# Performance work log

Measured on AMD Instinct MI355X. Metric: run time of the kernel, lower is better.

## Reference

```python
import jax, jax.numpy as jnp
import numpy as np

B, S, T, D, H, DF, E = 16, 1024, 512, 512, 8, 2048, 4
DH = D // H
EPS = 1e-5


def setup_inputs() -> dict:
    key = jax.random.key(0)
    ks = iter(jax.random.split(key, 64))

    def nrm(shape, scale=0.02):
        return jax.random.normal(next(ks), shape, dtype=jnp.float32) * scale

    inp = {
        "x": jax.random.normal(next(ks), (B, S, D), dtype=jnp.float32),
        "cross": jax.random.normal(next(ks), (B, T, D), dtype=jnp.float32),
    }
    for p in ("sa", "ca"):
        for w in ("wq", "wk", "wv", "wo"):
            inp[f"{p}_{w}"] = nrm((D, D))
            inp[f"{p}_b{w[1]}"] = jnp.zeros((D,), jnp.float32)
    inp["gate_w"] = nrm((D, E))
    inp["gate_b"] = jnp.zeros((E,), jnp.float32)
    inp["exp_w1"] = nrm((E, D, DF))
    inp["exp_b1"] = jnp.zeros((E, DF), jnp.float32)
    inp["exp_w2"] = nrm((E, DF, D))
    inp["exp_b2"] = jnp.zeros((E, D), jnp.float32)
    for i in (1, 2, 3):
        inp[f"n{i}_g"] = jnp.ones((D,), jnp.float32)
        inp[f"n{i}_b"] = jnp.zeros((D,), jnp.float32)
    return inp


def layer_norm(x, g, b):
    m = x.mean(-1, keepdims=True)
    v = x.var(-1, keepdims=True)
    return (x - m) * jax.lax.rsqrt(v + EPS) * g + b


def mha(q_in, kv_in, wq, bq, wk, bk, wv, bv, wo, bo, causal):
    Bq, Sq, _ = q_in.shape
    Sk = kv_in.shape[1]
    q = (q_in @ wq + bq).reshape(Bq, Sq, H, DH)
    k = (kv_in @ wk + bk).reshape(Bq, Sk, H, DH)
    v = (kv_in @ wv + bv).reshape(Bq, Sk, H, DH)
    scores = jnp.einsum('bshd,bthd->bhst', q, k) / jnp.sqrt(jnp.float32(DH))
    if causal:
        mask = jnp.tril(jnp.ones((Sq, Sk), dtype=bool))
        scores = jnp.where(mask, scores, jnp.float32(-1e9))
    attn = jax.nn.softmax(scores, axis=-1)
    out = jnp.einsum('bhst,bthd->bshd', attn, v).reshape(Bq, Sq, D)
    return out @ wo + bo


def moe_ffn(x, gw, gb, w1, b1, w2, b2):
    gates = jax.nn.softmax(x @ gw + gb, axis=-1)            # [B,S,E]
    h = jax.nn.relu(jnp.einsum('bsd,edf->bsef', x, w1) + b1)  # [B,S,E,DF]
    yo = jnp.einsum('bsef,efd->bsed', h, w2) + b2            # [B,S,E,D]
    y = jnp.einsum('bse,bsed->bsd', gates, yo)
    imp = gates.mean((0, 1))                                 # importance per expert
    aux = jnp.float32(E) * jnp.sum(imp * imp)                # load-balance penalty
    return y, aux


def reference(x, cross,
              sa_wq, sa_bq, sa_wk, sa_bk, sa_wv, sa_bv, sa_wo, sa_bo,
              ca_wq, ca_bq, ca_wk, ca_bk, ca_wv, ca_bv, ca_wo, ca_bo,
              gate_w, gate_b, exp_w1, exp_b1, exp_w2, exp_b2,
              n1_g, n1_b, n2_g, n2_b, n3_g, n3_b):
    # dropout is identity in eval mode
    x = x + mha(x, x, sa_wq, sa_bq, sa_wk, sa_bk, sa_wv, sa_bv, sa_wo, sa_bo, causal=True)
    x = layer_norm(x, n1_g, n1_b)
    x = x + mha(x, cross, ca_wq, ca_bq, ca_wk, ca_bk, ca_wv, ca_bv, ca_wo, ca_bo, causal=False)
    x = layer_norm(x, n2_g, n2_b)
    y, aux_loss = moe_ffn(x, gate_w, gate_b, exp_w1, exp_b1, exp_w2, exp_b2)
    out = layer_norm(x + y, n3_g, n3_b)
    return out, aux_loss
```

## Files before the change

kernel.cpp:

```cpp
#include <hip/hip_runtime.h>
#include <stdint.h>
#include <stddef.h>

typedef unsigned short bf16u;
typedef __attribute__((ext_vector_type(8))) short short8;
typedef __attribute__((ext_vector_type(4))) float f32x4;

__device__ __forceinline__ bf16u f2bf(float f) {
  union { float f; unsigned u; } v; v.f = f;
  unsigned r = v.u + 0x7FFFu + ((v.u >> 16) & 1u);
  return (bf16u)(r >> 16);
}

#define GL16(g, l) __builtin_amdgcn_global_load_lds( \
    (const __attribute__((address_space(1))) unsigned int*)(g), \
    (__attribute__((address_space(3))) unsigned int*)(l), 16, 0, 0)

enum { EPI_BF16 = 0, EPI_RELU_GATE = 1, EPI_VT = 2, EPI_RES = 3, EPI_ACC = 4 };

template<int EPI>
__global__ __launch_bounds__(256, 2) void gemm_k(
    const bf16u* __restrict__ A, const bf16u* __restrict__ BT,
    const float* __restrict__ bias, const float* __restrict__ res,
    const float* __restrict__ gates,
    bf16u* __restrict__ outb, float* __restrict__ outf,
    int M, int N, int K, int slog, int egate, int firste)
{
  __shared__ bf16u Ab[2][128 * 32];
  __shared__ bf16u Bb[2][128 * 32];
  const int tid = threadIdx.x, lane = tid & 63, w = tid >> 6;
  const int wm = w >> 1, wn = w & 1;
  const int nbt = N >> 7;
  const int mt = blockIdx.x / nbt, nt = blockIdx.x - mt * nbt;
  const int bm = mt << 7, bn = nt << 7;

  const int srow = lane >> 2;
  const int scol = (lane & 3) << 3;
  const bf16u* ap0 = A + (size_t)(bm + w * 16 + srow) * K + scol;
  const bf16u* ap1 = ap0 + (size_t)64 * K;
  const bf16u* bp0 = BT + (size_t)(bn + w * 16 + srow) * K + scol;
  const bf16u* bp1 = bp0 + (size_t)64 * K;

  f32x4 acc[4][4] = {};
  const int NT = K >> 5;

  GL16(ap0, &Ab[0][w * 512]);
  GL16(ap1, &Ab[0][(4 + w) * 512]);
  GL16(bp0, &Bb[0][w * 512]);
  GL16(bp1, &Bb[0][(4 + w) * 512]);
  __syncthreads();

  const int rl = lane & 15, kg = (lane >> 4) << 3;
  int cur = 0;
  for (int kt = 0; kt < NT; ++kt) {
    if (kt + 1 < NT) {
      const int ko = (kt + 1) << 5;
      const int nb = cur ^ 1;
      GL16(ap0 + ko, &Ab[nb][w * 512]);
      GL16(ap1 + ko, &Ab[nb][(4 + w) * 512]);
      GL16(bp0 + ko, &Bb[nb][w * 512]);
      GL16(bp1 + ko, &Bb[nb][(4 + w) * 512]);
    }
    short8 af[4], bfv[4];
    #pragma unroll
    for (int i = 0; i < 4; ++i)
      af[i] = *(const short8*)&Ab[cur][(wm * 64 + i * 16 + rl) * 32 + kg];
    #pragma unroll
    for (int j = 0; j < 4; ++j)
      bfv[j] = *(const short8*)&Bb[cur][(wn * 64 + j * 16 + rl) * 32 + kg];
    #pragma unroll
    for (int i = 0; i < 4; ++i)
      #pragma unroll
      for (int j = 0; j < 4; ++j)
        acc[i][j] = __builtin_amdgcn_mfma_f32_16x16x32_bf16(af[i], bfv[j], acc[i][j], 0, 0, 0);
    __syncthreads();
    cur ^= 1;
  }

  const int r0 = bm + wm * 64, c0 = bn + wn * 64;
  const int rsub = (lane >> 4) << 2;
  #pragma unroll
  for (int j = 0; j < 4; ++j) {
    const int col = c0 + j * 16 + rl;
    const float bs = bias ? bias[col] : 0.f;
    #pragma unroll
    for (int i = 0; i < 4; ++i) {
      const f32x4 v = acc[i][j];
      #pragma unroll
      for (int jj = 0; jj < 4; ++jj) {
        const int row = r0 + i * 16 + rsub + jj;
        float val = v[jj] + bs;
        if (EPI == EPI_BF16) {
          outb[(size_t)row * N + col] = f2bf(val);
        } else if (EPI == EPI_RELU_GATE) {
          const float g = gates[(size_t)row * 4 + egate];
          outb[(size_t)row * N + col] = f2bf(g * (val > 0.f ? val : 0.f));
        } else if (EPI == EPI_VT) {
          const int b_ = row >> slog, t_ = row & ((1 << slog) - 1);
          outb[(((size_t)(b_ * 8 + (col >> 6)) << 6) + (size_t)(col & 63)) * ((size_t)1 << slog) + t_] = f2bf(val);
        } else if (EPI == EPI_RES) {
          outf[(size_t)row * N + col] = res[(size_t)row * N + col] + val;
        } else {
          const size_t oi = (size_t)row * N + col;
          outf[oi] = firste ? val : (outf[oi] + val);
        }
      }
    }
  }
}

template<bool CAUSAL>
__global__ __launch_bounds__(256, 4) void attn_k(
    const bf16u* __restrict__ Q, const bf16u* __restrict__ Kg,
    const bf16u* __restrict__ VT, bf16u* __restrict__ O,
    int Sq, int Sk)
{
  __shared__ bf16u Kl[2][64 * 64];
  __shared__ bf16u Vl[2][64 * 64];
  __shared__ bf16u Pl[64 * 64];
  const int nqt = Sq >> 6;
  const int bh = blockIdx.x / nqt, qt = blockIdx.x - bh * nqt;
  const int b = bh >> 3, h = bh & 7;
  const int tid = threadIdx.x, lane = tid & 63, w = tid >> 6;
  const int rl = lane & 15, g4 = lane >> 4;

  const int qrow = qt * 64 + w * 16 + rl;
  const bf16u* qp = Q + (size_t)(b * Sq + qrow) * 512 + h * 64 + g4 * 8;
  const short8 qf0 = *(const short8*)qp;
  const short8 qf1 = *(const short8*)(qp + 32);

  f32x4 oacc[4] = {};
  float ml = -1e30f, ll = 0.f;
  const int KT = CAUSAL ? (qt + 1) : (Sk >> 6);

  const int str = tid >> 2, stc = tid & 3;
  const int sw_st = (str & 7) << 4;
  const bf16u* kq = Kg + (size_t)(b * Sk + str) * 512 + h * 64 + stc * 8;
  const bf16u* vq = VT + (size_t)(bh * 64 + str) * Sk + stc * 8;
  const int lo0 = str * 128 + ((stc * 16) ^ sw_st);
  const int lo1 = str * 128 + ((stc * 16 + 64) ^ sw_st);

  const int qr = w * 16 + rl;
  char* const pbase = (char*)Pl + qr * 128;
  const int swq = (qr & 7) << 4;

  {
    const short8 k0 = *(const short8*)kq;
    const short8 k1 = *(const short8*)(kq + 32);
    const short8 v0 = *(const short8*)vq;
    const short8 v1 = *(const short8*)(vq + 32);
    *(short8*)((char*)Kl[0] + lo0) = k0;
    *(short8*)((char*)Kl[0] + lo1) = k1;
    *(short8*)((char*)Vl[0] + lo0) = v0;
    *(short8*)((char*)Vl[0] + lo1) = v1;
  }
  __syncthreads();

  int cur = 0;
  for (int kt = 0; kt < KT; ++kt) {
    short8 nk0, nk1, nv0, nv1;
    const bool pre = (kt + 1 < KT);
    if (pre) {
      const bf16u* ks = kq + (size_t)(kt + 1) * 64 * 512;
      const bf16u* vs = vq + (kt + 1) * 64;
      nk0 = *(const short8*)ks;
      nk1 = *(const short8*)(ks + 32);
      nv0 = *(const short8*)vs;
      nv1 = *(const short8*)(vs + 32);
    }

    const bf16u* Kc = Kl[cur];
    const bf16u* Vc = Vl[cur];
    f32x4 st[4] = {};
    #pragma unroll
    for (int mi = 0; mi < 4; ++mi) {
      const int kr = mi * 16 + rl;
      const char* kb_ = (const char*)Kc + kr * 128;
      const int sw = (kr & 7) << 4;
      const short8 kf0 = *(const short8*)(kb_ + ((g4 * 16) ^ sw));
      const short8 kf1 = *(const short8*)(kb_ + ((g4 * 16 + 64) ^ sw));
      st[mi] = __builtin_amdgcn_mfma_f32_16x16x32_bf16(kf0, qf0, st[mi], 0, 0, 0);
      st[mi] = __builtin_amdgcn_mfma_f32_16x16x32_bf16(kf1, qf1, st[mi], 0, 0, 0);
    }

    const float SC = 0.125f * 1.44269504f;
    float sv[16];
    float pm = -1e30f;
    if (CAUSAL && kt == qt) {
      const int qg = qt * 64 + qr;
      #pragma unroll
      for (int mi = 0; mi < 4; ++mi)
        #pragma unroll
        for (int jj = 0; jj < 4; ++jj) {
          float s = st[mi][jj] * SC;
          const int kgi = kt * 64 + mi * 16 + g4 * 4 + jj;
          if (kgi > qg) s = -1e30f;
          sv[mi * 4 + jj] = s;
          pm = fmaxf(pm, s);
        }
    } else {
      #pragma unroll
      for (int mi = 0; mi < 4; ++mi)
        #pragma unroll
        for (int jj = 0; jj < 4; ++jj) {
          const float s = st[mi][jj] * SC;
          sv[mi * 4 + jj] = s;
          pm = fmaxf(pm, s);
        }
    }
    pm = fmaxf(pm, __shfl_xor(pm, 16));
    pm = fmaxf(pm, __shfl_xor(pm, 32));
    const float mnew = fmaxf(ml, pm);
    const float alpha = exp2f(ml - mnew);
    float ps = 0.f;
    bf16u pb[16];
    #pragma unroll
    for (int ii = 0; ii < 16; ++ii) {
      const float p = exp2f(sv[ii] - mnew);
      ps += p;
      pb[ii] = f2bf(p);
    }
    ps += __shfl_xor(ps, 16);
    ps += __shfl_xor(ps, 32);
    ll = ll * alpha + ps;
    ml = mnew;

    #pragma unroll
    for (int jj = 0; jj < 4; ++jj) {
      const float aj = __shfl(alpha, g4 * 4 + jj);
      #pragma unroll
      for (int ni = 0; ni < 4; ++ni) oacc[ni][jj] *= aj;
    }

    #pragma unroll
    for (int mi = 0; mi < 4; ++mi) {
      #pragma unroll
      for (int jp = 0; jp < 2; ++jp) {
        const unsigned pk = (unsigned)pb[mi * 4 + jp * 2] | ((unsigned)pb[mi * 4 + jp * 2 + 1] << 16);
        const int kx2 = mi * 32 + g4 * 8 + jp * 4;
        *(unsigned*)(pbase + (kx2 ^ swq)) = pk;
      }
    }
    asm volatile("s_waitcnt lgkmcnt(0)" ::: "memory");
    #pragma unroll
    for (int ks = 0; ks < 2; ++ks) {
      const short8 pf = *(const short8*)(pbase + ((g4 * 16 + ks * 64) ^ swq));
      #pragma unroll
      for (int ni = 0; ni < 4; ++ni) {
        const int vr = ni * 16 + rl;
        const short8 vf = *(const short8*)((const char*)Vc + vr * 128 + ((g4 * 16 + ks * 64) ^ ((vr & 7) << 4)));
        oacc[ni] = __builtin_amdgcn_mfma_f32_16x16x32_bf16(pf, vf, oacc[ni], 0, 0, 0);
      }
    }

    __syncthreads();
    if (pre) {
      const int nb = cur ^ 1;
      *(short8*)((char*)Kl[nb] + lo0) = nk0;
      *(short8*)((char*)Kl[nb] + lo1) = nk1;
      *(short8*)((char*)Vl[nb] + lo0) = nv0;
      *(short8*)((char*)Vl[nb] + lo1) = nv1;
      __syncthreads();
    }
    cur ^= 1;
  }

  #pragma unroll
  for (int jj = 0; jj < 4; ++jj) {
    const float lj = __shfl(ll, g4 * 4 + jj);
    const float inv = 1.f / lj;
    const int row = qt * 64 + w * 16 + g4 * 4 + jj;
    #pragma unroll
    for (int ni = 0; ni < 4; ++ni)
      O[(size_t)(b * Sq + row) * 512 + h * 64 + ni * 16 + rl] = f2bf(oacc[ni][jj] * inv);
  }
}

template<bool ADD, bool BOUT>
__global__ __launch_bounds__(256, 4) void ln_k(
    const float* __restrict__ X, const float* __restrict__ Y,
    const float* __restrict__ gam, const float* __restrict__ bet,
    float* __restrict__ outf, bf16u* __restrict__ outb)
{
  const int row = blockIdx.x * 4 + (threadIdx.x >> 6);
  const int lane = threadIdx.x & 63;
  const float* xp = X + (size_t)row * 512 + lane * 8;
  float v[8];
  {
    const float4 t0 = *(const float4*)xp;
    const float4 t1 = *(const float4*)(xp + 4);
    v[0] = t0.x; v[1] = t0.y; v[2] = t0.z; v[3] = t0.w;
    v[4] = t1.x; v[5] = t1.y; v[6] = t1.z; v[7] = t1.w;
  }
  if (ADD) {
    const float* yp = Y + (size_t)row * 512 + lane * 8;
    const float4 t0 = *(const float4*)yp;
    const float4 t1 = *(const float4*)(yp + 4);
    v[0] += t0.x; v[1] += t0.y; v[2] += t0.z; v[3] += t0.w;
    v[4] += t1.x; v[5] += t1.y; v[6] += t1.z; v[7] += t1.w;
  }
  float s = 0.f, q = 0.f;
  #pragma unroll
  for (int i = 0; i < 8; ++i) { s += v[i]; q += v[i] * v[i]; }
  #pragma unroll
  for (int off = 1; off < 64; off <<= 1) {
    s += __shfl_xor(s, off);
    q += __shfl_xor(q, off);
  }
  const float mean = s * (1.f / 512.f);
  const float var = q * (1.f / 512.f) - mean * mean;
  const float rs = rsqrtf(var + 1e-5f);
  float o[8];
  #pragma unroll
  for (int i = 0; i < 8; ++i) {
    const float g = gam[lane * 8 + i], bb = bet[lane * 8 + i];
    o[i] = (v[i] - mean) * rs * g + bb;
  }
  float* op = outf + (size_t)row * 512 + lane * 8;
  *(float4*)op = make_float4(o[0], o[1], o[2], o[3]);
  *(float4*)(op + 4) = make_float4(o[4], o[5], o[6], o[7]);
  if (BOUT) {
    union { bf16u u[8]; short8 v8; } pk;
    #pragma unroll
    for (int i = 0; i < 8; ++i) pk.u[i] = f2bf(o[i]);
    *(short8*)(outb + (size_t)row * 512 + lane * 8) = pk.v8;
  }
}

__global__ __launch_bounds__(256, 4) void ln_final_k(
    const float* __restrict__ X, const float* __restrict__ Y,
    const float* __restrict__ gates, const float* __restrict__ b2,
    const float* __restrict__ gam, const float* __restrict__ bet,
    float* __restrict__ outf)
{
  const int row = blockIdx.x * 4 + (threadIdx.x >> 6);
  const int lane = threadIdx.x & 63;
  const float4 gv4 = *(const float4*)(gates + (size_t)row * 4);
  float v[8];
  {
    const float* xp = X + (size_t)row * 512 + lane * 8;
    const float* yp = Y + (size_t)row * 512 + lane * 8;
    const float4 t0 = *(const float4*)xp;
    const float4 t1 = *(const float4*)(xp + 4);
    const float4 u0 = *(const float4*)yp;
    const float4 u1 = *(const float4*)(yp + 4);
    v[0] = t0.x + u0.x; v[1] = t0.y + u0.y; v[2] = t0.z + u0.z; v[3] = t0.w + u0.w;
    v[4] = t1.x + u1.x; v[5] = t1.y + u1.y; v[6] = t1.z + u1.z; v[7] = t1.w + u1.w;
  }
  #pragma unroll
  for (int e = 0; e < 4; ++e) {
    const float ge = e == 0 ? gv4.x : e == 1 ? gv4.y : e == 2 ? gv4.z : gv4.w;
    const float4 b0 = *(const float4*)(b2 + e * 512 + lane * 8);
    const float4 b1 = *(const float4*)(b2 + e * 512 + lane * 8 + 4);
    v[0] += ge * b0.x; v[1] += ge * b0.y; v[2] += ge * b0.z; v[3] += ge * b0.w;
    v[4] += ge * b1.x; v[5] += ge * b1.y; v[6] += ge * b1.z; v[7] += ge * b1.w;
  }
  float s = 0.f, q = 0.f;
  #pragma unroll
  for (int i = 0; i < 8; ++i) { s += v[i]; q += v[i] * v[i]; }
  #pragma unroll
  for (int off = 1; off < 64; off <<= 1) {
    s += __shfl_xor(s, off);
    q += __shfl_xor(q, off);
  }
  const float mean = s * (1.f / 512.f);
  const float var = q * (1.f / 512.f) - mean * mean;
  const float rs = rsqrtf(var + 1e-5f);
  float* op = outf + (size_t)row * 512 + lane * 8;
  float o[8];
  #pragma unroll
  for (int i = 0; i < 8; ++i)
    o[i] = (v[i] - mean) * rs * gam[lane * 8 + i] + bet[lane * 8 + i];
  *(float4*)op = make_float4(o[0], o[1], o[2], o[3]);
  *(float4*)(op + 4) = make_float4(o[4], o[5], o[6], o[7]);
}

__global__ __launch_bounds__(256, 4) void gate_k(
    const float* __restrict__ X, const float* __restrict__ gw,
    const float* __restrict__ gb, float* __restrict__ gates,
    float* __restrict__ imp)
{
  __shared__ float sh[4];
  const int tid = threadIdx.x;
  if (tid < 4) sh[tid] = 0.f;
  __syncthreads();
  const int row = blockIdx.x * 4 + (tid >> 6);
  const int lane = tid & 63;
  const float* xr = X + (size_t)row * 512;
  float a0 = 0.f, a1 = 0.f, a2 = 0.f, a3 = 0.f;
  for (int d = lane; d < 512; d += 64) {
    const float xv = xr[d];
    const float4 wv = *(const float4*)(gw + d * 4);
    a0 += xv * wv.x; a1 += xv * wv.y; a2 += xv * wv.z; a3 += xv * wv.w;
  }
  #pragma unroll
  for (int off = 1; off < 64; off <<= 1) {
    a0 += __shfl_xor(a0, off); a1 += __shfl_xor(a1, off);
    a2 += __shfl_xor(a2, off); a3 += __shfl_xor(a3, off);
  }
  if (lane == 0) {
    a0 += gb[0]; a1 += gb[1]; a2 += gb[2]; a3 += gb[3];
    const float m = fmaxf(fmaxf(a0, a1), fmaxf(a2, a3));
    const float e0 = exp2f((a0 - m) * 1.44269504f);
    const float e1 = exp2f((a1 - m) * 1.44269504f);
    const float e2 = exp2f((a2 - m) * 1.44269504f);
    const float e3 = exp2f((a3 - m) * 1.44269504f);
    const float inv = 1.f / (e0 + e1 + e2 + e3);
    float* gr = gates + (size_t)row * 4;
    const float g0 = e0 * inv, g1 = e1 * inv, g2 = e2 * inv, g3 = e3 * inv;
    gr[0] = g0; gr[1] = g1; gr[2] = g2; gr[3] = g3;
    atomicAdd(&sh[0], g0); atomicAdd(&sh[1], g1);
    atomicAdd(&sh[2], g2); atomicAdd(&sh[3], g3);
  }
  __syncthreads();
  if (tid < 4) atomicAdd(&imp[tid], sh[tid]);
}

__global__ void aux_k(const float* __restrict__ imp, float* __restrict__ out) {
  if (threadIdx.x == 0 && blockIdx.x == 0) {
    float s = 0.f;
    #pragma unroll
    for (int e = 0; e < 4; ++e) { const float v = imp[e] * (1.f / 16384.f); s += v * v; }
    out[0] = 4.f * s;
  }
}

__global__ __launch_bounds__(256, 4) void conv_k(const float* __restrict__ in, bf16u* __restrict__ out) {
  const size_t i = ((size_t)blockIdx.x * 256 + threadIdx.x) * 8;
  const float4 a = *(const float4*)(in + i);
  const float4 b = *(const float4*)(in + i + 4);
  union { bf16u u[8]; short8 v; } pk;
  pk.u[0] = f2bf(a.x); pk.u[1] = f2bf(a.y); pk.u[2] = f2bf(a.z); pk.u[3] = f2bf(a.w);
  pk.u[4] = f2bf(b.x); pk.u[5] = f2bf(b.y); pk.u[6] = f2bf(b.z); pk.u[7] = f2bf(b.w);
  *(short8*)(out + i) = pk.v;
}

__global__ __launch_bounds__(256, 4) void trans_k(
    const float* __restrict__ W, bf16u* __restrict__ WT, int K, int N)
{
  __shared__ float t[32][33];
  const int tx = threadIdx.x & 31, ty = threadIdx.x >> 5;
  const int n0 = blockIdx.x * 32, k0 = blockIdx.y * 32;
  #pragma unroll
  for (int i = 0; i < 4; ++i)
    t[ty + i * 8][tx] = W[(size_t)(k0 + ty + i * 8) * N + n0 + tx];
  __syncthreads();
  #pragma unroll
  for (int i = 0; i < 4; ++i)
    WT[(size_t)(n0 + ty + i * 8) * K + k0 + tx] = f2bf(t[tx][ty + i * 8]);
}

extern "C" void kernel_launch(void* const* d_in, const int* in_sizes, int n_in,
                              void* d_out, int out_size, void* d_ws, size_t ws_size,
                              hipStream_t stream)
{
  const int B = 16, S = 1024, T = 512, D = 512, DF = 2048, E = 4;
  const int M = B * S;
  const int Mc = B * T;
  (void)in_sizes; (void)n_in; (void)out_size; (void)ws_size;

  const float* x      = (const float*)d_in[0];
  const float* cross  = (const float*)d_in[1];
  const float* gate_w = (const float*)d_in[18];
  const float* gate_b = (const float*)d_in[19];
  const float* exp_w1 = (const float*)d_in[20];
  const float* exp_b1 = (const float*)d_in[21];
  const float* exp_w2 = (const float*)d_in[22];
  const float* exp_b2 = (const float*)d_in[23];

  char* p = (char*)d_ws;
  auto alloc = [&](size_t bytes) -> char* {
    char* r = p;
    p += (bytes + 255) & ~(size_t)255;
    return r;
  };
  bf16u* xb    = (bf16u*)alloc((size_t)M * D * 2);
  bf16u* crb   = (bf16u*)alloc((size_t)Mc * D * 2);
  bf16u* wT    = (bf16u*)alloc((size_t)8 * D * D * 2);
  bf16u* w1T   = (bf16u*)alloc((size_t)E * DF * D * 2);
  bf16u* w2T   = (bf16u*)alloc((size_t)E * D * DF * 2);
  bf16u* qb    = (bf16u*)alloc((size_t)M * D * 2);
  bf16u* kb    = (bf16u*)alloc((size_t)M * D * 2);
  bf16u* vTb   = (bf16u*)alloc((size_t)M * D * 2);
  bf16u* ao    = (bf16u*)alloc((size_t)M * D * 2);
  float* xf    = (float*)alloc((size_t)M * D * 4);
  bf16u* x2b   = (bf16u*)alloc((size_t)M * D * 2);
  float* gates = (float*)alloc((size_t)M * 4 * 4);
  float* imp   = (float*)alloc(256);
  bf16u* hbuf  = (bf16u*)alloc((size_t)M * DF * 2);
  float* y     = (float*)alloc((size_t)M * D * 4);

  hipMemsetAsync(imp, 0, 32, stream);
  conv_k<<<(M * D) / 2048, 256, 0, stream>>>(x, xb);
  conv_k<<<(Mc * D) / 2048, 256, 0, stream>>>(cross, crb);
  for (int i = 0; i < 8; ++i)
    trans_k<<<dim3(D / 32, D / 32), 256, 0, stream>>>((const float*)d_in[2 + 2 * i], wT + (size_t)i * D * D, D, D);
  for (int e = 0; e < E; ++e)
    trans_k<<<dim3(DF / 32, D / 32), 256, 0, stream>>>(exp_w1 + (size_t)e * D * DF, w1T + (size_t)e * DF * D, D, DF);
  for (int e = 0; e < E; ++e)
    trans_k<<<dim3(D / 32, DF / 32), 256, 0, stream>>>(exp_w2 + (size_t)e * DF * D, w2T + (size_t)e * D * DF, DF, D);

  const int gMD  = (M / 128) * (D / 128);
  const int gMcD = (Mc / 128) * (D / 128);
  const int gMDF = (M / 128) * (DF / 128);

  gemm_k<EPI_BF16><<<gMD, 256, 0, stream>>>(xb, wT + 0 * (size_t)D * D, (const float*)d_in[3], nullptr, nullptr, qb, nullptr, M, D, D, 0, 0, 0);
  gemm_k<EPI_BF16><<<gMD, 256, 0, stream>>>(xb, wT + 1 * (size_t)D * D, (const float*)d_in[5], nullptr, nullptr, kb, nullptr, M, D, D, 0, 0, 0);
  gemm_k<EPI_VT><<<gMD, 256, 0, stream>>>(xb, wT + 2 * (size_t)D * D, (const float*)d_in[7], nullptr, nullptr, vTb, nullptr, M, D, D, 10, 0, 0);
  attn_k<true><<<B * 8 * (S / 64), 256, 0, stream>>>(qb, kb, vTb, ao, S, S);
  gemm_k<EPI_RES><<<gMD, 256, 0, stream>>>(ao, wT + 3 * (size_t)D * D, (const float*)d_in[9], x, nullptr, nullptr, xf, M, D, D, 0, 0, 0);
  ln_k<false, true><<<M / 4, 256, 0, stream>>>(xf, nullptr, (const float*)d_in[24], (const float*)d_in[25], xf, x2b);

  gemm_k<EPI_BF16><<<gMD, 256, 0, stream>>>(x2b, wT + 4 * (size_t)D * D, (const float*)d_in[11], nullptr, nullptr, qb, nullptr, M, D, D, 0, 0, 0);
  gemm_k<EPI_BF16><<<gMcD, 256, 0, stream>>>(crb, wT + 5 * (size_t)D * D, (const float*)d_in[13], nullptr, nullptr, kb, nullptr, Mc, D, D, 0, 0, 0);
  gemm_k<EPI_VT><<<gMcD, 256, 0, stream>>>(crb, wT + 6 * (size_t)D * D, (const float*)d_in[15], nullptr, nullptr, vTb, nullptr, Mc, D, D, 9, 0, 0);
  attn_k<false><<<B * 8 * (S / 64), 256, 0, stream>>>(qb, kb, vTb, ao, S, T);
  gemm_k<EPI_RES><<<gMD, 256, 0, stream>>>(ao, wT + 7 * (size_t)D * D, (const float*)d_in[17], xf, nullptr, nullptr, xf, M, D, D, 0, 0, 0);
  ln_k<false, true><<<M / 4, 256, 0, stream>>>(xf, nullptr, (const float*)d_in[26], (const float*)d_in[27], xf, x2b);

  gate_k<<<M / 4, 256, 0, stream>>>(xf, gate_w, gate_b, gates, imp);
  aux_k<<<1, 64, 0, stream>>>(imp, (float*)d_out + (size_t)M * D);
  for (int e = 0; e < E; ++e) {
    gemm_k<EPI_RELU_GATE><<<gMDF, 256, 0, stream>>>(x2b, w1T + (size_t)e * DF * D, exp_b1 + (size_t)e * DF, nullptr, gates, hbuf, nullptr, M, DF, D, 0, e, 0);
    gemm_k<EPI_ACC><<<gMD, 256, 0, stream>>>(hbuf, w2T + (size_t)e * D * DF, nullptr, nullptr, nullptr, nullptr, y, M, D, DF, 0, 0, e == 0 ? 1 : 0);
  }
  ln_final_k<<<M / 4, 256, 0, stream>>>(xf, y, gates, exp_b2, (const float*)d_in[28], (const float*)d_in[29], (float*)d_out);
}
```

Baseline: 1.010 ms.

## Fuse QKV and KV projection GEMMs, batch MoE experts into wide GEMMs, swizzle block order

The self-attention Q, K and V projections now run as one GEMM with N=1536, and the cross-attention K and V projections as one GEMM with N=1024. The epilogue routes each column range to its own output buffer, including the transposed V layout. The MoE expert loop is regrouped so that when workspace allows, all experts' first layers run as a single wide GEMM and the second layers as a single K=8192 GEMM accumulated in fp32, which removes per-expert launches and read-modify-write passes on y. A blockIdx remap across groups of 8 is added, likely to spread neighbouring tiles across XCDs, and a larger workspace is needed for the hidden buffer.

```diff
diff --git a/kernel.cpp b/kernel.cpp
--- a/kernel.cpp
+++ b/kernel.cpp
@@ -16,30 +16,34 @@
     (const __attribute__((address_space(1))) unsigned int*)(g), \
     (__attribute__((address_space(3))) unsigned int*)(l), 16, 0, 0)
 
-enum { EPI_BF16 = 0, EPI_RELU_GATE = 1, EPI_VT = 2, EPI_RES = 3, EPI_ACC = 4 };
+enum { EPI_BF16 = 0, EPI_RELU_GATE = 1, EPI_QKV = 2, EPI_RES = 3, EPI_F32ACC = 4, EPI_KV = 5 };
 
 template<int EPI>
 __global__ __launch_bounds__(256, 2) void gemm_k(
-    const bf16u* __restrict__ A, const bf16u* __restrict__ BT,
+    const bf16u* __restrict__ A, int LDA,
+    const bf16u* __restrict__ BT, int LDB,
     const float* __restrict__ bias, const float* __restrict__ res,
     const float* __restrict__ gates,
-    bf16u* __restrict__ outb, float* __restrict__ outf,
-    int M, int N, int K, int slog, int egate, int firste)
+    bf16u* __restrict__ o1, bf16u* __restrict__ o2, bf16u* __restrict__ o3,
+    float* __restrict__ of,
+    int N, int K, int slog, int egate0, int firste)
 {
   __shared__ bf16u Ab[2][128 * 32];
   __shared__ bf16u Bb[2][128 * 32];
   const int tid = threadIdx.x, lane = tid & 63, w = tid >> 6;
   const int wm = w >> 1, wn = w & 1;
+  const int cpx = gridDim.x >> 3;
+  const int bid = (blockIdx.x & 7) * cpx + (blockIdx.x >> 3);
   const int nbt = N >> 7;
-  const int mt = blockIdx.x / nbt, nt = blockIdx.x - mt * nbt;
+  const int mt = bid / nbt, nt = bid - mt * nbt;
   const int bm = mt << 7, bn = nt << 7;
 
   const int srow = lane >> 2;
   const int scol = (lane & 3) << 3;
-  const bf16u* ap0 = A + (size_t)(bm + w * 16 + srow) * K + scol;
-  const bf16u* ap1 = ap0 + (size_t)64 * K;
-  const bf16u* bp0 = BT + (size_t)(bn + w * 16 + srow) * K + scol;
-  const bf16u* bp1 = bp0 + (size_t)64 * K;
+  const bf16u* ap0 = A + (size_t)(bm + w * 16 + srow) * LDA + scol;
+  const bf16u* ap1 = ap0 + (size_t)64 * LDA;
+  const bf16u* bp0 = BT + (size_t)(bn + w * 16 + srow) * LDB + scol;
+  const bf16u* bp1 = bp0 + (size_t)64 * LDB;
 
   f32x4 acc[4][4] = {};
   const int NT = K >> 5;
@@ -89,20 +93,32 @@
       #pragma unroll
       for (int jj = 0; jj < 4; ++jj) {
         const int row = r0 + i * 16 + rsub + jj;
-        float val = v[jj] + bs;
+        const float val = v[jj] + bs;
         if (EPI == EPI_BF16) {
-          outb[(size_t)row * N + col] = f2bf(val);
+          o1[(size_t)row * N + col] = f2bf(val);
         } else if (EPI == EPI_RELU_GATE) {
-          const float g = gates[(size_t)row * 4 + egate];
-          outb[(size_t)row * N + col] = f2bf(g * (val > 0.f ? val : 0.f));
-        } else if (EPI == EPI_VT) {
-          const int b_ = row >> slog, t_ = row & ((1 << slog) - 1);
-          outb[(((size_t)(b_ * 8 + (col >> 6)) << 6) + (size_t)(col & 63)) * ((size_t)1 << slog) + t_] = f2bf(val);
+          const float g = gates[(size_t)row * 4 + egate0 + (col >> 11)];
+          o1[(size_t)row * N + col] = f2bf(g * (val > 0.f ? val : 0.f));
+        } else if (EPI == EPI_QKV) {
+          if (col < 512) o1[(size_t)row * 512 + col] = f2bf(val);
+          else if (col < 1024) o2[(size_t)row * 512 + col - 512] = f2bf(val);
+          else {
+            const int c = col - 1024;
+            const int b_ = row >> slog, t_ = row & ((1 << slog) - 1);
+            o3[(((size_t)(b_ * 8 + (c >> 6)) << 6) + (size_t)(c & 63)) * ((size_t)1 << slog) + t_] = f2bf(val);
+          }
+        } else if (EPI == EPI_KV) {
+          if (col < 512) o2[(size_t)row * 512 + col] = f2bf(val);
+          else {
+            const int c = col - 512;
+            const int b_ = row >> slog, t_ = row & ((1 << slog) - 1);
+            o3[(((size_t)(b_ * 8 + (c >> 6)) << 6) + (size_t)(c & 63)) * ((size_t)1 << slog) + t_] = f2bf(val);
+          }
         } else if (EPI == EPI_RES) {
-          outf[(size_t)row * N + col] = res[(size_t)row * N + col] + val;
+          of[(size_t)row * N + col] = res[(size_t)row * N + col] + val;
         } else {
           const size_t oi = (size_t)row * N + col;
-          outf[oi] = firste ? val : (outf[oi] + val);
+          of[oi] = firste ? val : (of[oi] + val);
         }
       }
     }
@@ -457,7 +473,7 @@
   const int B = 16, S = 1024, T = 512, D = 512, DF = 2048, E = 4;
   const int M = B * S;
   const int Mc = B * T;
-  (void)in_sizes; (void)n_in; (void)out_size; (void)ws_size;
+  (void)in_sizes; (void)n_in; (void)out_size;
 
   const float* x      = (const float*)d_in[0];
   const float* cross  = (const float*)d_in[1];
@@ -478,7 +494,7 @@
   bf16u* crb   = (bf16u*)alloc((size_t)Mc * D * 2);
   bf16u* wT    = (bf16u*)alloc((size_t)8 * D * D * 2);
   bf16u* w1T   = (bf16u*)alloc((size_t)E * DF * D * 2);
-  bf16u* w2T   = (bf16u*)alloc((size_t)E * D * DF * 2);
+  bf16u* w2T   = (bf16u*)alloc((size_t)D * E * DF * 2);
   bf16u* qb    = (bf16u*)alloc((size_t)M * D * 2);
   bf16u* kb    = (bf16u*)alloc((size_t)M * D * 2);
   bf16u* vTb   = (bf16u*)alloc((size_t)M * D * 2);
@@ -487,42 +503,64 @@
   bf16u* x2b   = (bf16u*)alloc((size_t)M * D * 2);
   float* gates = (float*)alloc((size_t)M * 4 * 4);
   float* imp   = (float*)alloc(256);
-  bf16u* hbuf  = (bf16u*)alloc((size_t)M * DF * 2);
   float* y     = (float*)alloc((size_t)M * D * 4);
+  float* qkvb  = (float*)alloc(1536 * 4);
+  float* kvb   = (float*)alloc(1024 * 4);
+
+  const size_t used = (size_t)(p - (char*)d_ws);
+  const size_t perE = (size_t)M * DF * 2;
+  const size_t rem = ws_size > used ? ws_size - used : 0;
+  const int EC = rem >= 4 * perE + 4096 ? 4 : rem >= 2 * perE + 4096 ? 2 : 1;
+  bf16u* hbuf = (bf16u*)alloc((size_t)EC * perE);
 
   hipMemsetAsync(imp, 0, 32, stream);
+  hipMemcpyAsync(qkvb,        d_in[3], 512 * 4, hipMemcpyDeviceToDevice, stream);
+  hipMemcpyAsync(qkvb + 512,  d_in[5], 512 * 4, hipMemcpyDeviceToDevice, stream);
+  hipMemcpyAsync(qkvb + 1024, d_in[7], 512 * 4, hipMemcpyDeviceToDevice, stream);
+  hipMemcpyAsync(kvb,         d_in[13], 512 * 4, hipMemcpyDeviceToDevice, stream);
+  hipMemcpyAsync(kvb + 512,   d_in[15], 512 * 4, hipMemcpyDeviceToDevice, stream);
+
   conv_k<<<(M * D) / 2048, 256, 0, stream>>>(x, xb);
   conv_k<<<(Mc * D) / 2048, 256, 0, stream>>>(cross, crb);
   for (int i = 0; i < 8; ++i)
     trans_k<<<dim3(D / 32, D / 32), 256, 0, stream>>>((const float*)d_in[2 + 2 * i], wT + (size_t)i * D * D, D, D);
   for (int e = 0; e < E; ++e)
     trans_k<<<dim3(DF / 32, D / 32), 256, 0, stream>>>(exp_w1 + (size_t)e * D * DF, w1T + (size_t)e * DF * D, D, DF);
-  for (int e = 0; e < E; ++e)
-    trans_k<<<dim3(D / 32, DF / 32), 256, 0, stream>>>(exp_w2 + (size_t)e * DF * D, w2T + (size_t)e * D * DF, DF, D);
-
-  const int gMD  = (M / 128) * (D / 128);
-  const int gMcD = (Mc / 128) * (D / 128);
-  const int gMDF = (M / 128) * (DF / 128);
-
-  gemm_k<EPI_BF16><<<gMD, 256, 0, stream>>>(xb, wT + 0 * (size_t)D * D, (const float*)d_in[3], nullptr, nullptr, qb, nullptr, M, D, D, 0, 0, 0);
-  gemm_k<EPI_BF16><<<gMD, 256, 0, stream>>>(xb, wT + 1 * (size_t)D * D, (const float*)d_in[5], nullptr, nullptr, kb, nullptr, M, D, D, 0, 0, 0);
-  gemm_k<EPI_VT><<<gMD, 256, 0, stream>>>(xb, wT + 2 * (size_t)D * D, (const float*)d_in[7], nullptr, nullptr, vTb, nullptr, M, D, D, 10, 0, 0);
-  attn_k<true><<<B * 8 * (S / 64), 256, 0, stream>>>(qb, kb, vTb, ao, S, S);
-  gemm_k<EPI_RES><<<gMD, 256, 0, stream>>>(ao, wT + 3 * (size_t)D * D, (const float*)d_in[9], x, nullptr, nullptr, xf, M, D, D, 0, 0, 0);
+  trans_k<<<dim3(D / 32, (E * DF) / 32), 256, 0, stream>>>(exp_w2, w2T, E * DF, D);
+
+  const int gATT = B * 8 * (S / 64);
+
+  gemm_k<EPI_QKV><<<(M / 128) * 12, 256, 0, stream>>>(
+      xb, 512, wT, 512, qkvb, nullptr, nullptr, qb, kb, vTb, nullptr, 1536, 512, 10, 0, 0);
+  attn_k<true><<<gATT, 256, 0, stream>>>(qb, kb, vTb, ao, S, S);
+  gemm_k<EPI_RES><<<(M / 128) * 4, 256, 0, stream>>>(
+      ao, 512, wT + 3 * (size_t)D * D, 512, (const float*)d_in[9], x, nullptr,
+      nullptr, nullptr, nullptr, xf, 512, 512, 0, 0, 0);
   ln_k<false, true><<<M / 4, 256, 0, stream>>>(xf, nullptr, (const float*)d_in[24], (const float*)d_in[25], xf, x2b);
 
-  gemm_k<EPI_BF16><<<gMD, 256, 0, stream>>>(x2b, wT + 4 * (size_t)D * D, (const float*)d_in[11], nullptr, nullptr, qb, nullptr, M, D, D, 0, 0, 0);
-  gemm_k<EPI_BF16><<<gMcD, 256, 0, stream>>>(crb, wT + 5 * (size_t)D * D, (const float*)d_in[13], nullptr, nullptr, kb, nullptr, Mc, D, D, 0, 0, 0);
-  gemm_k<EPI_VT><<<gMcD, 256, 0, stream>>>(crb, wT + 6 * (size_t)D * D, (const float*)d_in[15], nullptr, nullptr, vTb, nullptr, Mc, D, D, 9, 0, 0);
-  attn_k<false><<<B * 8 * (S / 64), 256, 0, stream>>>(qb, kb, vTb, ao, S, T);
-  gemm_k<EPI_RES><<<gMD, 256, 0, stream>>>(ao, wT + 7 * (size_t)D * D, (const float*)d_in[17], xf, nullptr, nullptr, xf, M, D, D, 0, 0, 0);
+  gemm_k<EPI_BF16><<<(M / 128) * 4, 256, 0, stream>>>(
+      x2b, 512, wT + 4 * (size_t)D * D, 512, (const float*)d_in[11], nullptr, nullptr,
+      qb, nullptr, nullptr, nullptr, 512, 512, 0, 0, 0);
+  gemm_k<EPI_KV><<<(Mc / 128) * 8, 256, 0, stream>>>(
+      crb, 512, wT + 5 * (size_t)D * D, 512, kvb, nullptr, nullptr,
+      nullptr, kb, vTb, nullptr, 1024, 512, 9, 0, 0);
+  attn_k<false><<<gATT, 256, 0, stream>>>(qb, kb, vTb, ao, S, T);
+  gemm_k<EPI_RES><<<(M / 128) * 4, 256, 0, stream>>>(
+      ao, 512, wT + 7 * (size_t)D * D, 512, (const float*)d_in[17], xf, nullptr,
+      nullptr, nullptr, nullptr, xf, 512, 512, 0, 0, 0);
   ln_k<false, true><<<M / 4, 256, 0, stream>>>(xf, nullptr, (const float*)d_in[26], (const float*)d_in[27], xf, x2b);
 
   gate_k<<<M / 4, 256, 0, stream>>>(xf, gate_w, gate_b, gates, imp);
   aux_k<<<1, 64, 0, stream>>>(imp, (float*)d_out + (size_t)M * D);
-  for (int e = 0; e < E; ++e) {
-    gemm_k<EPI_RELU_GATE><<<gMDF, 256, 0, stream>>>(x2b, w1T + (size_t)e * DF * D, exp_b1 + (size_t)e * DF, nullptr, gates, hbuf, nullptr, M, DF, D, 0, e, 0);
-    gemm_k<EPI_ACC><<<gMD, 256, 0, stream>>>(hbuf, w2T + (size_t)e * D * DF, nullptr, nullptr, nullptr, nullptr, y, M, D, DF, 0, 0, e == 0 ? 1 : 0);
+  const int NC = E / EC;
+  const int Nh = EC * DF;
+  for (int c = 0; c < NC; ++c) {
+    gemm_k<EPI_RELU_GATE><<<(M / 128) * (Nh / 128), 256, 0, stream>>>(
+        x2b, 512, w1T + (size_t)c * Nh * D, 512, exp_b1 + (size_t)c * Nh, nullptr, gates,
+        hbuf, nullptr, nullptr, nullptr, Nh, 512, 0, c * EC, 0);
+    gemm_k<EPI_F32ACC><<<(M / 128) * 4, 256, 0, stream>>>(
+        hbuf, Nh, w2T + (size_t)c * Nh, E * DF, nullptr, nullptr, nullptr,
+        nullptr, nullptr, nullptr, y, 512, Nh, 0, 0, c == 0 ? 1 : 0);
   }
   ln_final_k<<<M / 4, 256, 0, stream>>>(xf, y, gates, exp_b2, (const float*)d_in[28], (const float*)d_in[29], (float*)d_out);
 }
```

After: 962.3 us. 4.7% less time.
